# Optimization experiments

Hardware: AMD Instinct MI355X
Metric: run time of the kernel (lower is better)

Reference implementation:

```python
import jax, jax.numpy as jnp
import numpy as np


def _pool_mat(N, pn):
    # F.interpolate(mode='area') == adaptive_avg_pool1d: output i averages
    # input indices [floor(i*N/pn), ceil((i+1)*N/pn))
    W = np.zeros((pn, N), dtype=np.float32)
    for i in range(pn):
        s = (i * N) // pn
        e = -((-(i + 1) * N) // pn)  # ceil((i+1)*N/pn)
        W[i, s:e] = 1.0 / (e - s)
    return W


def _up_mat(pn, N):
    # F.interpolate(mode='linear', align_corners=False) from length pn to N
    W = np.zeros((N, pn), dtype=np.float32)
    scale = pn / N
    for j in range(N):
        pos = max((j + 0.5) * scale - 0.5, 0.0)
        i0 = min(int(np.floor(pos)), pn - 1)
        i1 = min(i0 + 1, pn - 1)
        frac = pos - i0
        W[j, i0] += 1.0 - frac
        W[j, i1] += frac
    return W


def setup_inputs() -> dict:
    key = jax.random.key(0)
    k1, k2 = jax.random.split(key)
    B, N, C, K = 512, 16, 256, 8192
    f = jax.random.normal(k1, (B, N, C), dtype=jnp.float32)
    # original init: uniform(-1/K, 1/K)
    emb = jax.random.uniform(k2, (K, C), dtype=jnp.float32, minval=-1.0 / K, maxval=1.0 / K)
    return {"f": f, "emb": emb}


def reference(f, emb):
    B, N, C = f.shape
    fT = jnp.transpose(f, (0, 2, 1))            # [B, C, N]
    f_ng = jax.lax.stop_gradient(fT)
    emb_ng = jax.lax.stop_gradient(emb)
    e_sq = jnp.sum(emb_ng * emb_ng, axis=1)     # [K]
    f_rest = f_ng
    f_hat = jnp.zeros_like(f_ng)
    commit = jnp.float32(0.0)
    qlat = jnp.float32(0.0)
    for pn in range(1, N + 1):
        rest_bcn = jax.lax.stop_gradient(f_rest)
        if pn < N:
            Wp = jnp.asarray(_pool_mat(N, pn))             # [pn, N]
            rest = jnp.einsum('pn,bcn->bpc', Wp, rest_bcn).reshape(-1, C)
        else:
            rest = jnp.transpose(rest_bcn, (0, 2, 1)).reshape(-1, C)
        # squared euclidean distances [B*pn, K]
        d = jnp.sum(rest * rest, axis=1, keepdims=True) + e_sq - 2.0 * (rest @ emb_ng.T)
        idx = jnp.argmin(d, axis=1).reshape(B, pn)
        h = jnp.transpose(emb[idx], (0, 2, 1))             # [B, C, pn]
        if pn < N:
            Wu = jnp.asarray(_up_mat(pn, N))               # [N, pn]
            h = jnp.einsum('np,bcp->bcn', Wu, h)
        f_hat = f_hat + h
        f_rest = f_rest - h
        commit = commit + 0.25 * jnp.mean((jax.lax.stop_gradient(f_hat) - fT) ** 2)
        qlat = qlat + jnp.mean((f_hat - f_ng) ** 2)
    commit = commit / N
    qlat = qlat / N
    # straight-through estimator
    f_hat_out = jax.lax.stop_gradient(f_hat) - f_ng + fT
    return jnp.transpose(f_hat_out, (0, 2, 1)), commit, qlat
```

## Files before the change

kernel.cpp:

```cpp
#include <hip/hip_runtime.h>
#include <math.h>

#define BB 512
#define NN 16
#define CC 256
#define KK 8192
#define BNC (BB*NN*CC)

typedef unsigned short u16;
typedef __attribute__((ext_vector_type(8))) short bf16x8;
typedef __attribute__((ext_vector_type(4))) float f32x4;

__device__ __forceinline__ u16 f2bf(float x) {
    unsigned u = __float_as_uint(x);
    unsigned r = (u + 0x7fffu + ((u >> 16) & 1u)) >> 16;
    return (u16)r;
}

__device__ __forceinline__ void gl2lds16(const void* g, void* l) {
    __builtin_amdgcn_global_load_lds(
        (const __attribute__((address_space(1))) void*)g,
        (__attribute__((address_space(3))) void*)l,
        16, 0, 0);
}

__device__ __forceinline__ void gl2lds4(const void* g, void* l) {
    __builtin_amdgcn_global_load_lds(
        (const __attribute__((address_space(1))) void*)g,
        (__attribute__((address_space(3))) void*)l,
        4, 0, 0);
}

__global__ void esq_cvt_kernel(const float* __restrict__ emb,
                               float* __restrict__ e_sq,
                               u16* __restrict__ out) {
    int gid = blockIdx.x * blockDim.x + threadIdx.x;
    int lane = gid & 63;
    float4 v = ((const float4*)emb)[gid];
    ushort4 o;
    o.x = f2bf(-v.x); o.y = f2bf(-v.y); o.z = f2bf(-v.z); o.w = f2bf(-v.w);
    ((ushort4*)out)[gid] = o;
    float s = v.x*v.x + v.y*v.y + v.z*v.z + v.w*v.w;
    #pragma unroll
    for (int m = 32; m >= 1; m >>= 1) s += __shfl_xor(s, m, 64);
    if (lane == 0) e_sq[gid >> 6] = 0.5f * s;
}

__global__ void init_pool_kernel(const float* __restrict__ f,
                                 u16* __restrict__ rest_bf) {
    int b = blockIdx.x;
    int c = threadIdx.x;
    const float* base = f + (size_t)b * NN * CC + c;
    float acc = 0.f;
    #pragma unroll
    for (int n = 0; n < NN; ++n) acc += base[(size_t)n * CC];
    rest_bf[(size_t)b * CC + c] = f2bf(acc * (1.0f / 16.0f));
}

__device__ __forceinline__ unsigned long long shfl_xor_u64(unsigned long long v, int m) {
    unsigned lo = (unsigned)v, hi = (unsigned)(v >> 32);
    lo = __shfl_xor(lo, m, 64);
    hi = __shfl_xor(hi, m, 64);
    return ((unsigned long long)hi << 32) | lo;
}

__global__ __launch_bounds__(512, 2) void dist_mfma_kernel(
        const u16* __restrict__ A, const u16* __restrict__ Bm,
        const float* __restrict__ e_sq,
        unsigned long long* __restrict__ packed, int cpb) {
    __shared__ __align__(16) u16 sC[32768];
    __shared__ __align__(16) float sE[512];
    const int tid = threadIdx.x;
    const int w = tid >> 6, l = tid & 63;
    const int r0 = blockIdx.x * 256;
    const int c0 = blockIdx.y * cpb;
    const int ncb2 = cpb >> 6;
    const int arow = l & 15;
    const int aq   = l >> 4;

    bf16x8 bf[2][8];
    {
        const u16* fb = A + (((size_t)(r0 + w * 32 + arow)) << 8) + aq * 8;
        #pragma unroll
        for (int j = 0; j < 2; ++j)
            #pragma unroll
            for (int kc = 0; kc < 8; ++kc)
                bf[j][kc] = *(const bf16x8*)(fb + (j << 12) + (kc << 5));
    }

    for (int n = tid; n < cpb; n += 512)
        gl2lds4(e_sq + c0 + n, (char*)sE + (size_t)(n - l) * 4);

    const int g = (l & 3) ^ ((l >> 3) & 3);
    const u16* Pb = Bm + (((size_t)(c0 + (l >> 2))) << 8) + g * 8;

    #define STAGE_CB(cb_) { \
        const u16* s0_ = Pb + ((size_t)(cb_) << 14) + (w << 5); \
        char* d0_ = (char*)sC + (((cb_) & 1) << 15) + (w << 12); \
        _Pragma("unroll") \
        for (int i_ = 0; i_ < 4; ++i_) \
            gl2lds16(s0_ + (i_ << 12), d0_ + (i_ << 10)); }

    STAGE_CB(0)

    const int gx = aq ^ ((arow >> 1) & 3);
    float bestd[2];
    int   bestk[2];
    #pragma unroll
    for (int j = 0; j < 2; ++j) { bestd[j] = 1e30f; bestk[j] = 0; }

    asm volatile("s_waitcnt vmcnt(0)" ::: "memory");
    __builtin_amdgcn_s_barrier();
    asm volatile("" ::: "memory");

    for (int cb = 0; cb < ncb2; ++cb) {
        if (cb + 1 < ncb2) STAGE_CB(cb + 1)

        f32x4 acc[4][2];
        #pragma unroll
        for (int i = 0; i < 4; ++i) {
            f32x4 ev = *(const f32x4*)(sE + cb * 64 + i * 16 + (aq << 2));
            #pragma unroll
            for (int j = 0; j < 2; ++j) acc[i][j] = ev;
        }

        const u16* bufp = sC + ((cb & 1) << 14);
        #pragma unroll
        for (int c = 0; c < 8; ++c) {
            bf16x8 cf[4];
            const u16* cbp = bufp + (c << 11);
            #pragma unroll
            for (int i = 0; i < 4; ++i)
                cf[i] = *(const bf16x8*)(cbp + ((i * 16 + arow) << 5) + (gx << 3));
            #pragma unroll
            for (int i = 0; i < 4; ++i)
                #pragma unroll
                for (int j = 0; j < 2; ++j)
                    acc[i][j] = __builtin_amdgcn_mfma_f32_16x16x32_bf16(
                                    cf[i], bf[j][c], acc[i][j], 0, 0, 0);
        }

        #pragma unroll
        for (int i = 0; i < 4; ++i)
            #pragma unroll
            for (int r = 0; r < 4; ++r) {
                const int k = c0 + cb * 64 + i * 16 + (aq << 2) + r;
                #pragma unroll
                for (int j = 0; j < 2; ++j) {
                    const float d = acc[i][j][r];
                    if (d < bestd[j]) { bestd[j] = d; bestk[j] = k; }
                }
            }

        asm volatile("s_waitcnt vmcnt(0) lgkmcnt(0)" ::: "memory");
        __builtin_amdgcn_s_barrier();
        asm volatile("" ::: "memory");
    }
    #undef STAGE_CB

    #pragma unroll
    for (int j = 0; j < 2; ++j) {
        unsigned u = __float_as_uint(bestd[j]);
        u = (u & 0x80000000u) ? ~u : (u | 0x80000000u);
        unsigned long long p = ((unsigned long long)u << 32) | (unsigned)bestk[j];
        unsigned long long o = shfl_xor_u64(p, 16);
        if (o < p) p = o;
        o = shfl_xor_u64(p, 32);
        if (o < p) p = o;
        if (aq == 0)
            atomicMin(&packed[r0 + w * 32 + j * 16 + arow], p);
    }
}

__global__ void update_pool_kernel(const float* __restrict__ f,
                                   const float* __restrict__ emb,
                                   const unsigned long long* __restrict__ packed,
                                   float* __restrict__ f_rest,
                                   float* __restrict__ out,
                                   float* __restrict__ slots,
                                   u16* __restrict__ rest_bf, int pn) {
    int b = blockIdx.x;
    int c = threadIdx.x;
    __shared__ int sk[NN];
    __shared__ float red[4];
    if (threadIdx.x < pn)
        sk[threadIdx.x] = (int)(unsigned)(packed[b * pn + threadIdx.x] & 0xffffffffull);
    __syncthreads();

    float fr[NN];
    float acc_sq = 0.f;
    #pragma unroll
    for (int n = 0; n < NN; ++n) {
        double pos = (n + 0.5) * ((double)pn / 16.0) - 0.5;
        if (pos < 0.0) pos = 0.0;
        int i0 = (int)floor(pos);
        if (i0 > pn - 1) i0 = pn - 1;
        int i1 = i0 + 1;
        if (i1 > pn - 1) i1 = pn - 1;
        double frac = pos - (double)i0;
        float w1 = (float)frac;
        float w0 = (float)(1.0 - frac);
        float h = w0 * emb[(size_t)sk[i0] * CC + c] + w1 * emb[(size_t)sk[i1] * CC + c];
        size_t off = ((size_t)b * NN + n) * CC + c;
        float fre = f_rest[off] - h;
        fr[n] = fre;
        acc_sq += fre * fre;
        if (pn < NN) {
            f_rest[off] = fre;
        } else {
            out[off] = f[off] - fre;
        }
    }

    int wv = threadIdx.x >> 6, ln = threadIdx.x & 63;
    #pragma unroll
    for (int m = 32; m >= 1; m >>= 1) acc_sq += __shfl_xor(acc_sq, m, 64);
    if (ln == 0) red[wv] = acc_sq;

    int pn2 = pn + 1;
    if (pn < NN) {
        for (int p = 0; p < pn2; ++p) {
            int s = (p * NN) / pn2;
            int e = ((p + 1) * NN + pn2 - 1) / pn2;
            float v = 0.f;
            for (int n = s; n < e; ++n) v += fr[n];
            v *= 1.0f / (float)(e - s);
            rest_bf[((size_t)(b * pn2 + p)) * CC + c] = f2bf(v);
        }
    }
    __syncthreads();
    if (threadIdx.x == 0)
        atomicAdd(&slots[b & 255], (red[0] + red[1]) + (red[2] + red[3]));
}

__global__ void final_kernel(const float* __restrict__ slots, float* __restrict__ out_scalars) {
    float v = slots[threadIdx.x];
    #pragma unroll
    for (int m = 32; m >= 1; m >>= 1) v += __shfl_xor(v, m, 64);
    __shared__ float red[4];
    int wv = threadIdx.x >> 6, ln = threadIdx.x & 63;
    if (ln == 0) red[wv] = v;
    __syncthreads();
    if (threadIdx.x == 0) {
        float S = (red[0] + red[1]) + (red[2] + red[3]);
        float qlat = S / (float)BNC / (float)NN;
        out_scalars[0] = 0.25f * qlat;
        out_scalars[1] = qlat;
    }
}

extern "C" void kernel_launch(void* const* d_in, const int* in_sizes, int n_in,
                              void* d_out, int out_size, void* d_ws, size_t ws_size,
                              hipStream_t stream) {
    (void)in_sizes; (void)n_in; (void)out_size; (void)ws_size;
    const float* f   = (const float*)d_in[0];
    const float* emb = (const float*)d_in[1];
    float* out = (float*)d_out;

    float* ws      = (float*)d_ws;
    float* f_rest  = ws;
    float* r2_pad  = f_rest + BNC;
    float* e_sq    = r2_pad + BB * NN;
    float* slots   = e_sq + KK;
    unsigned long long* packed_all = (unsigned long long*)(slots + 256);
    u16* rest_bf = (u16*)(packed_all + (size_t)BB * 136);
    u16* emb_bf  = rest_bf + (size_t)BB * NN * CC;

    hipMemcpyAsync(f_rest, f, (size_t)BNC * sizeof(float), hipMemcpyDeviceToDevice, stream);
    hipMemsetAsync(slots, 0, 256 * sizeof(float), stream);
    hipMemsetAsync(packed_all, 0xFF, (size_t)BB * 136 * sizeof(unsigned long long), stream);
    esq_cvt_kernel<<<KK * CC / 4 / 256, 256, 0, stream>>>(emb, e_sq, emb_bf);
    init_pool_kernel<<<BB, 256, 0, stream>>>(f, rest_bf);

    static const int splits_tab[17] =
        {0,128,128,128,64,64,64,64,32,32,32,32,32,32,32,32,16};

    for (int pn = 1; pn <= NN; ++pn) {
        unsigned long long* packed = packed_all + (size_t)BB * (pn * (pn - 1) / 2);
        int splits = splits_tab[pn];
        int cpb = KK / splits;
        dim3 grid(BB * pn / 256, splits);
        dist_mfma_kernel<<<grid, 512, 0, stream>>>(rest_bf, emb_bf, e_sq, packed, cpb);
        update_pool_kernel<<<BB, 256, 0, stream>>>(f, emb, packed, f_rest, out,
                                                   slots, rest_bf, pn);
    }
    final_kernel<<<1, 256, 0, stream>>>(slots, out + BNC);
}
```

Before: 662.7 us.

## Deepen codebook LDS pipeline to a 16-slot ring with fine-grained chunk staging

Replaces the double-buffered per-64-code staging with a 16-slot ring of 8-code-column chunks. Each phase issues one chunk pair ahead and waits only until six loads remain outstanding, so several chunks stay in flight while MFMAs consume earlier ones. The aim is to hide global-to-LDS latency better than the old full vmcnt(0) wait per block. In exchange there are more barriers per block, and correctness depends on the ring depth and the clamped tail loads staying in step with the wait counts.

```diff
diff --git a/kernel.cpp b/kernel.cpp
--- a/kernel.cpp
+++ b/kernel.cpp
@@ -74,6 +74,7 @@
     const int w = tid >> 6, l = tid & 63;
     const int r0 = blockIdx.x * 256;
     const int c0 = blockIdx.y * cpb;
+    const int nch = cpb >> 3;
     const int ncb2 = cpb >> 6;
     const int arow = l & 15;
     const int aq   = l >> 4;
@@ -91,17 +92,19 @@
     for (int n = tid; n < cpb; n += 512)
         gl2lds4(e_sq + c0 + n, (char*)sE + (size_t)(n - l) * 4);
 
-    const int g = (l & 3) ^ ((l >> 3) & 3);
-    const u16* Pb = Bm + (((size_t)(c0 + (l >> 2))) << 8) + g * 8;
-
-    #define STAGE_CB(cb_) { \
-        const u16* s0_ = Pb + ((size_t)(cb_) << 14) + (w << 5); \
-        char* d0_ = (char*)sC + (((cb_) & 1) << 15) + (w << 12); \
-        _Pragma("unroll") \
-        for (int i_ = 0; i_ < 4; ++i_) \
-            gl2lds16(s0_ + (i_ << 12), d0_ + (i_ << 10)); }
-
-    STAGE_CB(0)
+    const int crel = (tid & 255) >> 2;
+    const int g = (tid & 3) ^ ((tid >> 3) & 3);
+    const u16* Pb = Bm + (((size_t)(c0 + crel)) << 8) + g * 8;
+
+    #define STAGE_PAIR(pp_) { \
+        int tc_ = ((pp_) << 1) + (tid >> 8); \
+        const int td_ = tc_ & 15; \
+        if (tc_ >= nch) tc_ = nch - 1; \
+        const u16* s_ = Pb + (((size_t)(tc_ >> 3)) << 14) + ((tc_ & 7) << 5); \
+        gl2lds16(s_, (char*)sC + (td_ << 12) + ((w & 3) << 10)); }
+
+    STAGE_PAIR(0) STAGE_PAIR(1) STAGE_PAIR(2)
+    STAGE_PAIR(3) STAGE_PAIR(4) STAGE_PAIR(5)
 
     const int gx = aq ^ ((arow >> 1) & 3);
     float bestd[2];
@@ -109,35 +112,37 @@
     #pragma unroll
     for (int j = 0; j < 2; ++j) { bestd[j] = 1e30f; bestk[j] = 0; }
 
-    asm volatile("s_waitcnt vmcnt(0)" ::: "memory");
-    __builtin_amdgcn_s_barrier();
-    asm volatile("" ::: "memory");
-
+    f32x4 acc[4][2];
     for (int cb = 0; cb < ncb2; ++cb) {
-        if (cb + 1 < ncb2) STAGE_CB(cb + 1)
-
-        f32x4 acc[4][2];
         #pragma unroll
-        for (int i = 0; i < 4; ++i) {
-            f32x4 ev = *(const f32x4*)(sE + cb * 64 + i * 16 + (aq << 2));
+        for (int ph = 0; ph < 4; ++ph) {
+            const int t = cb * 8 + ph * 2;
+            STAGE_PAIR((t >> 1) + 6)
+            asm volatile("s_waitcnt vmcnt(6)" ::: "memory");
+            __builtin_amdgcn_s_barrier();
+            if (ph == 0) {
+                #pragma unroll
+                for (int i = 0; i < 4; ++i) {
+                    f32x4 ev = *(const f32x4*)(sE + cb * 64 + i * 16 + (aq << 2));
+                    #pragma unroll
+                    for (int j = 0; j < 2; ++j) acc[i][j] = ev;
+                }
+            }
             #pragma unroll
-            for (int j = 0; j < 2; ++j) acc[i][j] = ev;
-        }
-
-        const u16* bufp = sC + ((cb & 1) << 14);
-        #pragma unroll
-        for (int c = 0; c < 8; ++c) {
-            bf16x8 cf[4];
-            const u16* cbp = bufp + (c << 11);
-            #pragma unroll
-            for (int i = 0; i < 4; ++i)
-                cf[i] = *(const bf16x8*)(cbp + ((i * 16 + arow) << 5) + (gx << 3));
-            #pragma unroll
-            for (int i = 0; i < 4; ++i)
-                #pragma unroll
-                for (int j = 0; j < 2; ++j)
-                    acc[i][j] = __builtin_amdgcn_mfma_f32_16x16x32_bf16(
-                                    cf[i], bf[j][c], acc[i][j], 0, 0, 0);
+            for (int h = 0; h < 2; ++h) {
+                const int kc = ph * 2 + h;
+                const u16* cbp = sC + (((t + h) & 15) << 11);
+                bf16x8 cf[4];
+                #pragma unroll
+                for (int i = 0; i < 4; ++i)
+                    cf[i] = *(const bf16x8*)(cbp + ((i * 16 + arow) << 5) + (gx << 3));
+                #pragma unroll
+                for (int i = 0; i < 4; ++i)
+                    #pragma unroll
+                    for (int j = 0; j < 2; ++j)
+                        acc[i][j] = __builtin_amdgcn_mfma_f32_16x16x32_bf16(
+                                        cf[i], bf[j][kc], acc[i][j], 0, 0, 0);
+            }
         }
 
         #pragma unroll
@@ -151,12 +156,8 @@
                     if (d < bestd[j]) { bestd[j] = d; bestk[j] = k; }
                 }
             }
-
-        asm volatile("s_waitcnt vmcnt(0) lgkmcnt(0)" ::: "memory");
-        __builtin_amdgcn_s_barrier();
-        asm volatile("" ::: "memory");
-    }
-    #undef STAGE_CB
+    }
+    #undef STAGE_PAIR
 
     #pragma unroll
     for (int j = 0; j < 2; ++j) {
```

Result: slower. 689.4 us (+4.0%).

## Template distance kernel on rows per warp, using 4-row-tile blocks for larger scales

Applied to the files above, without the earlier changes.

The MFMA distance/argmin kernel is templated on J, the number of 16-row tiles each warp holds in registers. For scales pn>=8 a J=4 variant is launched, so each block covers 512 rows instead of 256 and the grid shrinks to match. This makes each staged codebook tile in LDS serve twice as many query rows, roughly halving codebook global and LDS traffic per row. The cost is much higher register use (accumulators and A fragments double) under the same launch bounds, which risks spills or lower occupancy. The J=4 variant also declares a larger LDS buffer, which further limits blocks per CU.

```diff
diff --git a/kernel.cpp b/kernel.cpp
--- a/kernel.cpp
+++ b/kernel.cpp
@@ -64,25 +64,27 @@
     return ((unsigned long long)hi << 32) | lo;
 }
 
+template <int J>
 __global__ __launch_bounds__(512, 2) void dist_mfma_kernel(
         const u16* __restrict__ A, const u16* __restrict__ Bm,
         const float* __restrict__ e_sq,
         unsigned long long* __restrict__ packed, int cpb) {
-    __shared__ __align__(16) u16 sC[32768];
+    constexpr int SCSIZE = (J == 4) ? 41984 : 32768;
+    __shared__ __align__(16) u16 sC[SCSIZE];
     __shared__ __align__(16) float sE[512];
     const int tid = threadIdx.x;
     const int w = tid >> 6, l = tid & 63;
-    const int r0 = blockIdx.x * 256;
+    const int r0 = blockIdx.x * (128 * J);
     const int c0 = blockIdx.y * cpb;
     const int ncb2 = cpb >> 6;
     const int arow = l & 15;
     const int aq   = l >> 4;
 
-    bf16x8 bf[2][8];
+    bf16x8 bf[J][8];
     {
-        const u16* fb = A + (((size_t)(r0 + w * 32 + arow)) << 8) + aq * 8;
+        const u16* fb = A + (((size_t)(r0 + w * 16 * J + arow)) << 8) + aq * 8;
         #pragma unroll
-        for (int j = 0; j < 2; ++j)
+        for (int j = 0; j < J; ++j)
             #pragma unroll
             for (int kc = 0; kc < 8; ++kc)
                 bf[j][kc] = *(const bf16x8*)(fb + (j << 12) + (kc << 5));
@@ -104,10 +106,10 @@
     STAGE_CB(0)
 
     const int gx = aq ^ ((arow >> 1) & 3);
-    float bestd[2];
-    int   bestk[2];
-    #pragma unroll
-    for (int j = 0; j < 2; ++j) { bestd[j] = 1e30f; bestk[j] = 0; }
+    float bestd[J];
+    int   bestk[J];
+    #pragma unroll
+    for (int j = 0; j < J; ++j) { bestd[j] = 1e30f; bestk[j] = 0; }
 
     asm volatile("s_waitcnt vmcnt(0)" ::: "memory");
     __builtin_amdgcn_s_barrier();
@@ -116,12 +118,12 @@
     for (int cb = 0; cb < ncb2; ++cb) {
         if (cb + 1 < ncb2) STAGE_CB(cb + 1)
 
-        f32x4 acc[4][2];
+        f32x4 acc[4][J];
         #pragma unroll
         for (int i = 0; i < 4; ++i) {
             f32x4 ev = *(const f32x4*)(sE + cb * 64 + i * 16 + (aq << 2));
             #pragma unroll
-            for (int j = 0; j < 2; ++j) acc[i][j] = ev;
+            for (int j = 0; j < J; ++j) acc[i][j] = ev;
         }
 
         const u16* bufp = sC + ((cb & 1) << 14);
@@ -135,7 +137,7 @@
             #pragma unroll
             for (int i = 0; i < 4; ++i)
                 #pragma unroll
-                for (int j = 0; j < 2; ++j)
+                for (int j = 0; j < J; ++j)
                     acc[i][j] = __builtin_amdgcn_mfma_f32_16x16x32_bf16(
                                     cf[i], bf[j][c], acc[i][j], 0, 0, 0);
         }
@@ -146,7 +148,7 @@
             for (int r = 0; r < 4; ++r) {
                 const int k = c0 + cb * 64 + i * 16 + (aq << 2) + r;
                 #pragma unroll
-                for (int j = 0; j < 2; ++j) {
+                for (int j = 0; j < J; ++j) {
                     const float d = acc[i][j][r];
                     if (d < bestd[j]) { bestd[j] = d; bestk[j] = k; }
                 }
@@ -159,7 +161,7 @@
     #undef STAGE_CB
 
     #pragma unroll
-    for (int j = 0; j < 2; ++j) {
+    for (int j = 0; j < J; ++j) {
         unsigned u = __float_as_uint(bestd[j]);
         u = (u & 0x80000000u) ? ~u : (u | 0x80000000u);
         unsigned long long p = ((unsigned long long)u << 32) | (unsigned)bestk[j];
@@ -168,7 +170,7 @@
         o = shfl_xor_u64(p, 32);
         if (o < p) p = o;
         if (aq == 0)
-            atomicMin(&packed[r0 + w * 32 + j * 16 + arow], p);
+            atomicMin(&packed[r0 + w * 16 * J + j * 16 + arow], p);
     }
 }
 
@@ -272,15 +274,25 @@
     esq_cvt_kernel<<<KK * CC / 4 / 256, 256, 0, stream>>>(emb, e_sq, emb_bf);
     init_pool_kernel<<<BB, 256, 0, stream>>>(f, rest_bf);
 
-    static const int splits_tab[17] =
-        {0,128,128,128,64,64,64,64,32,32,32,32,32,32,32,32,16};
+    static const int splits_tab2[8] = {0, 128, 128, 128, 64, 64, 64, 64};
+    static const int splits_tab4[17] =
+        {0,0,0,0,0,0,0,0, 32,32,32,32,32,32,32,32, 16};
 
     for (int pn = 1; pn <= NN; ++pn) {
         unsigned long long* packed = packed_all + (size_t)BB * (pn * (pn - 1) / 2);
-        int splits = splits_tab[pn];
-        int cpb = KK / splits;
-        dim3 grid(BB * pn / 256, splits);
-        dist_mfma_kernel<<<grid, 512, 0, stream>>>(rest_bf, emb_bf, e_sq, packed, cpb);
+        if (pn < 8) {
+            int splits = splits_tab2[pn];
+            int cpb = KK / splits;
+            dim3 grid(BB * pn / 256, splits);
+            dist_mfma_kernel<2><<<grid, 512, 0, stream>>>(rest_bf, emb_bf, e_sq,
+                                                          packed, cpb);
+        } else {
+            int splits = splits_tab4[pn];
+            int cpb = KK / splits;
+            dim3 grid(BB * pn / 512, splits);
+            dist_mfma_kernel<4><<<grid, 512, 0, stream>>>(rest_bf, emb_bf, e_sq,
+                                                          packed, cpb);
+        }
         update_pool_kernel<<<BB, 256, 0, stream>>>(f, emb, packed, f_rest, out,
                                                    slots, rest_bf, pn);
     }
```

Measured after the change: 737.1 us. 11.2% more time.
